# Kernel optimization log

Measured on AMD Instinct MI355X. Metric: run time of the kernel, lower is better.

## Reference

```python
import jax, jax.numpy as jnp
import numpy as np

N_NODES = 20000
N_EDGES = 320000
N_GRAPHS = 512
HEADS1 = 10
C1 = 78   # per-head out channels of gcn1
C2 = 100  # out channels of gcn2 (heads=1)
NEG_SLOPE = 0.2


def setup_inputs() -> dict:
    key = jax.random.key(0)
    ks = jax.random.split(key, 16)
    glorot = lambda k, shp: jax.random.normal(k, shp, jnp.float32) * np.sqrt(2.0 / (shp[0] + shp[-1]))
    x = jax.random.normal(ks[0], (N_NODES, 78), jnp.float32)
    edge_index = jax.random.randint(ks[1], (2, N_EDGES), 0, N_NODES, jnp.int64)
    batch = jnp.sort(jax.random.randint(ks[2], (N_NODES,), 0, N_GRAPHS, jnp.int64))
    return {
        "x": x,
        "edge_index": edge_index,
        "batch": batch,
        "num_graphs": N_GRAPHS,
        "W1": glorot(ks[3], (78, HEADS1 * C1)),
        "a_src1": glorot(ks[4], (HEADS1, C1)),
        "a_dst1": glorot(ks[5], (HEADS1, C1)),
        "b1": jnp.zeros((HEADS1 * C1,), jnp.float32),
        "W2": glorot(ks[6], (HEADS1 * C1, C2)),
        "a_src2": glorot(ks[7], (1, C2)),
        "a_dst2": glorot(ks[8], (1, C2)),
        "b2": jnp.zeros((C2,), jnp.float32),
        "Wg": glorot(ks[9], (C2, C2)),
        "bg": jnp.zeros((C2,), jnp.float32),
    }


def gat_conv(x, src, dst, W, a_src, a_dst, b, heads, out_ch):
    """PyG-style GATConv (concat=True, add_self_loops already applied, eval mode)."""
    N = x.shape[0]
    h = (x @ W).reshape(N, heads, out_ch)          # [N,H,C]
    alpha_s = jnp.einsum('nhc,hc->nh', h, a_src)   # [N,H]
    alpha_d = jnp.einsum('nhc,hc->nh', h, a_dst)
    e = jax.nn.leaky_relu(alpha_s[src] + alpha_d[dst], NEG_SLOPE)  # [E,H]
    # segment softmax over destination nodes
    m = jax.ops.segment_max(e, dst, num_segments=N)                # [N,H]
    e = jnp.exp(e - m[dst])
    denom = jax.ops.segment_sum(e, dst, num_segments=N)
    alpha = e / (denom[dst] + 1e-16)                               # [E,H]
    out = jax.ops.segment_sum(h[src] * alpha[:, :, None], dst, num_segments=N)
    return out.reshape(N, heads * out_ch) + b


def reference(x, edge_index, batch, num_graphs, W1, a_src1, a_dst1, b1,
              W2, a_src2, a_dst2, b2, Wg, bg):
    N = x.shape[0]
    # add self loops (PyG GATConv default)
    loops = jnp.arange(N, dtype=edge_index.dtype)
    src = jnp.concatenate([edge_index[0], loops])
    dst = jnp.concatenate([edge_index[1], loops])
    h = gat_conv(x, src, dst, W1, a_src1, a_dst1, b1, HEADS1, C1)   # [N,780]
    h = jax.nn.elu(h)
    h = gat_conv(h, src, dst, W2, a_src2, a_dst2, b2, 1, C2)        # [N,100]
    h = jax.nn.relu(h)
    g = jax.ops.segment_max(h, batch, num_segments=num_graphs)      # [G,100] global max pool
    g = jax.nn.relu(g @ Wg + bg)
    return g
```

## Files before the change

### kernel.cpp

```cpp
#include <hip/hip_runtime.h>
#include <hip/hip_bf16.h>

#define N_NODES  20000
#define N_EDGES  320000
#define E_TOT    (N_EDGES + N_NODES)
#define N_GRAPHS 512
#define H1 10
#define C1 78
#define F1 780
#define C2 100
#define NEG_SLOPE 0.2f
#define KSPLIT 5
#define K1PAD 96
#define K2PAD 800
#define K2CHUNK 160
#define AP1 104
#define AP2 40
#define HP 12

typedef short bf16x8 __attribute__((ext_vector_type(8)));
typedef float f32x4 __attribute__((ext_vector_type(4)));
typedef _Float16 half2v __attribute__((ext_vector_type(2)));
typedef unsigned short ushort_t;

__device__ __forceinline__ float bf_lo(unsigned int u) { return __uint_as_float(u << 16); }
__device__ __forceinline__ float bf_hi(unsigned int u) { return __uint_as_float(u & 0xFFFF0000u); }
__device__ __forceinline__ ushort_t f2b(float v) {
  __hip_bfloat16 b = __float2bfloat16(v);
  return *reinterpret_cast<ushort_t*>(&b);
}
__device__ __forceinline__ ushort_t f2h(float v) {
  _Float16 h = (_Float16)v;
  return *reinterpret_cast<ushort_t*>(&h);
}
__device__ __forceinline__ float lrelu(float v) { return (v > 0.f) ? v : NEG_SLOPE * v; }
__device__ __forceinline__ float dot2h(unsigned int a, unsigned int b, float c) {
  union { unsigned int u; half2v v; } A, B;
  A.u = a; B.u = b;
  return __builtin_amdgcn_fdot2(A.v, B.v, c, false);
}


#define PR0 (2 * H1 * C1)
#define PR1 (H1 * 80 * K1PAD)
#define PR2 (112 * K2PAD)
#define PR3 (N_NODES * (K2PAD - F1))
#define PR4 (N_NODES * 40)
#define PRT (PR0 + PR1 + PR2 + PR3 + PR4)
#define NB_CNT ((E_TOT + 255) / 256)
#define NB_PREP ((PRT + 255) / 256)

__global__ void k_cntprep(const int* __restrict__ ei,
                          const float* __restrict__ W1, const float* __restrict__ a_src,
                          const float* __restrict__ a_dst, const float* __restrict__ W2,
                          const float* __restrict__ x,
                          int* __restrict__ cnt,
                          float* __restrict__ Vs, float* __restrict__ Vd,
                          ushort_t* __restrict__ W1t, ushort_t* __restrict__ W2t,
                          ushort_t* __restrict__ hab, ushort_t* __restrict__ xhf) {
  if (blockIdx.x < NB_CNT) {
    int e = blockIdx.x * 256 + threadIdx.x;
    if (e >= E_TOT) return;
    int dst = (e < N_EDGES) ? ei[N_EDGES + e] : (e - N_EDGES);
    atomicAdd(&cnt[dst], 1);
    return;
  }
  int t = (blockIdx.x - NB_CNT) * 256 + threadIdx.x;
  if (t < PR0) {
    int which = (t >= H1 * C1) ? 1 : 0;
    int r = t - which * H1 * C1;
    int h = r / C1, k = r - h * C1;
    const float* a = which ? a_dst : a_src;
    float s = 0.f;
    for (int c = 0; c < C1; c++) s += W1[(size_t)k * F1 + h * C1 + c] * a[h * C1 + c];
    (which ? Vd : Vs)[h * C1 + k] = s;
    return;
  }
  t -= PR0;
  if (t < PR1) {
    int h = t / (80 * K1PAD);
    int rem = t - h * 80 * K1PAD;
    int c = rem / K1PAD, k = rem - c * K1PAD;
    float v = (c < C1 && k < C1) ? W1[(size_t)k * F1 + h * C1 + c] : 0.f;
    W1t[t] = f2b(v);
    return;
  }
  t -= PR1;
  if (t < PR2) {
    int c = t / K2PAD, k = t - c * K2PAD;
    float v = (c < C2 && k < F1) ? W2[(size_t)k * C2 + c] : 0.f;
    W2t[t] = f2b(v);
    return;
  }
  t -= PR2;
  if (t < PR3) {
    int n = t / (K2PAD - F1), j = t - n * (K2PAD - F1);
    hab[(size_t)n * K2PAD + F1 + j] = 0;
    return;
  }
  t -= PR3;
  if (t < PR4) {
    int n = t / 40, c2 = t - n * 40;
    ushort2 o;
    if (c2 < 39) { o.x = f2h(x[(size_t)n * C1 + 2 * c2]); o.y = f2h(x[(size_t)n * C1 + 2 * c2 + 1]); }
    else         { o.x = 0; o.y = 0; }
    *(ushort2*)(xhf + (size_t)n * 80 + 2 * c2) = o;
  }
}


__global__ __launch_bounds__(1024) void k_scanalpha(const int* __restrict__ cnt,
                                                    int* __restrict__ offs,
                                                    const float* __restrict__ x,
                                                    const float* __restrict__ Vs,
                                                    const float* __restrict__ Vd,
                                                    float* __restrict__ asb,
                                                    float* __restrict__ adb) {
  if (blockIdx.x == 0) {
    const int PER = 20;
    int t = threadIdx.x;
    int lane = t & 63, wv = t >> 6;
    int base = t * PER;
    int raw[PER];
    const int4* c4 = (const int4*)(cnt + base);
#pragma unroll
    for (int q = 0; q < 5; q++) {
      int4 v = c4[q];
      raw[4 * q] = v.x; raw[4 * q + 1] = v.y; raw[4 * q + 2] = v.z; raw[4 * q + 3] = v.w;
    }
    int loc[PER];
    int run = 0;
#pragma unroll
    for (int k = 0; k < PER; k++) {
      int idx = base + k;
      run += (idx < N_NODES) ? raw[k] : 0;
      loc[k] = run;
    }
    int total = run;
    int sc = total;
#pragma unroll
    for (int o = 1; o < 64; o <<= 1) {
      int u = __shfl_up(sc, o);
      if (lane >= o) sc += u;
    }
    __shared__ int ws[16];
    if (lane == 63) ws[wv] = sc;
    __syncthreads();
    if (t == 0) {
      int r = 0;
#pragma unroll
      for (int i = 0; i < 16; i++) { int v = ws[i]; ws[i] = r; r += v; }
    }
    __syncthreads();
    int excl = ws[wv] + sc - total;
#pragma unroll
    for (int k = 0; k < PER; k++) {
      int idx = base + k;
      if (idx < N_NODES) offs[idx + 1] = excl + loc[k];
    }
    if (t == 0) offs[0] = 0;
    return;
  }

  __shared__ float sVs[H1 * C1], sVd[H1 * C1];
  for (int i = threadIdx.x; i < H1 * C1; i += 1024) { sVs[i] = Vs[i]; sVd[i] = Vd[i]; }
  __syncthreads();
  int t = (blockIdx.x - 1) * 1024 + threadIdx.x;
  if (t >= N_NODES * H1) return;
  int n = t / H1, h = t - n * H1;
  const float2* row = (const float2*)(x + (size_t)n * C1);
  const float2* vs2 = (const float2*)(sVs + h * C1);
  const float2* vd2 = (const float2*)(sVd + h * C1);
  float s0 = 0.f, s1 = 0.f;
#pragma unroll 13
  for (int i = 0; i < C1 / 2; i++) {
    float2 v = row[i];
    float2 a = vs2[i];
    float2 b = vd2[i];
    s0 += v.x * a.x + v.y * a.y;
    s1 += v.x * b.x + v.y * b.y;
  }
  asb[(size_t)n * HP + h] = s0;
  adb[(size_t)n * HP + h] = s1;
}

__global__ void k_scatter(const int* __restrict__ ei, const int* __restrict__ offs,
                          int* __restrict__ cursor, int* __restrict__ srcs,
                          int* __restrict__ dsts) {
  int e = blockIdx.x * blockDim.x + threadIdx.x;
  if (e >= E_TOT) return;
  int src, dst;
  if (e < N_EDGES) { src = ei[e]; dst = ei[N_EDGES + e]; }
  else             { src = dst = e - N_EDGES; }
  int pos = offs[dst] + atomicAdd(&cursor[dst], 1);
  srcs[pos] = src;
  dsts[pos] = dst;
}


__global__ void k_ex1(const float* __restrict__ asb, const float* __restrict__ adb,
                      const int* __restrict__ srcs, const int* __restrict__ dsts,
                      ushort_t* __restrict__ ex1t) {
  int e = blockIdx.x * blockDim.x + threadIdx.x;
  if (e >= E_TOT) return;
  int s = srcs[e], d = dsts[e];
  const float* pa = asb + (size_t)s * HP;
  const float* pd = adb + (size_t)d * HP;
  float4 a0 = *(const float4*)pa, a1 = *(const float4*)(pa + 4);
  float2 a2 = *(const float2*)(pa + 8);
  float4 d0 = *(const float4*)pd, d1 = *(const float4*)(pd + 4);
  float2 d2 = *(const float2*)(pd + 8);
  float r[10];
  r[0] = __expf(lrelu(a0.x + d0.x)); r[1] = __expf(lrelu(a0.y + d0.y));
  r[2] = __expf(lrelu(a0.z + d0.z)); r[3] = __expf(lrelu(a0.w + d0.w));
  r[4] = __expf(lrelu(a1.x + d1.x)); r[5] = __expf(lrelu(a1.y + d1.y));
  r[6] = __expf(lrelu(a1.z + d1.z)); r[7] = __expf(lrelu(a1.w + d1.w));
  r[8] = __expf(lrelu(a2.x + d2.x)); r[9] = __expf(lrelu(a2.y + d2.y));
#pragma unroll
  for (int h = 0; h < H1; h++) ex1t[(size_t)h * E_TOT + e] = f2h(r[h]);
}


__global__ __launch_bounds__(256) void k_aggv5(const ushort_t* __restrict__ xhf,
                                               const ushort_t* __restrict__ ex1t,
                                               const int* __restrict__ offs,
                                               const int* __restrict__ srcs,
                                               ushort_t* __restrict__ xb) {
  int wid = (blockIdx.x * 256 + threadIdx.x) >> 6;
  int lane = threadIdx.x & 63;
  if (wid >= N_NODES) return;
  int n = wid;
  int beg = __builtin_amdgcn_readfirstlane(offs[n]);
  int end = __builtin_amdgcn_readfirstlane(offs[n + 1]);

  float acc0[H1] = {}, acc1[H1] = {}, sum[H1] = {};
  const unsigned int ONES = 0x3C003C00u;

  for (int e0 = beg & ~1; e0 < end; e0 += 2) {
    unsigned int m = 0xFFFFFFFFu;
    if (e0 < beg) m &= 0xFFFF0000u;
    if (e0 + 1 >= end) m &= 0x0000FFFFu;
    int s0 = srcs[e0], s1 = srcs[e0 + 1];
    unsigned int w[H1];
#pragma unroll
    for (int h = 0; h < H1; h++)
      w[h] = *(const unsigned int*)(ex1t + (size_t)h * E_TOT + e0);
    unsigned int xv0 = 0, xv1 = 0;
    if (lane < 39) {
      xv0 = *(const unsigned int*)(xhf + (size_t)s0 * 80 + 2 * lane);
      xv1 = *(const unsigned int*)(xhf + (size_t)s1 * 80 + 2 * lane);
    }
    unsigned int xA = __builtin_amdgcn_perm(xv1, xv0, 0x05040100u) & m;
    unsigned int xB = __builtin_amdgcn_perm(xv1, xv0, 0x07060302u) & m;
    unsigned int on = ONES & m;
#pragma unroll
    for (int h = 0; h < H1; h++) {
      acc0[h] = dot2h(w[h], xA, acc0[h]);
      acc1[h] = dot2h(w[h], xB, acc1[h]);
      sum[h]  = dot2h(w[h], on, sum[h]);
    }
  }

  if (lane < 48) {
    int colu = (lane < 39) ? 2 * lane : C1 + 2 * (lane - 39);
#pragma unroll
    for (int h = 0; h < H1; h++) {
      float iv = 1.f / (sum[h] + 1e-16f);
      ushort2 o;
      if (lane < 39) { o.x = f2b(acc0[h] * iv); o.y = f2b(acc1[h] * iv); }
      else           { o.x = 0; o.y = 0; }
      *(ushort2*)(xb + ((size_t)h * N_NODES + n) * K1PAD + colu) = o;
    }
  }
}


__global__ __launch_bounds__(256) void k_bgemm_m(const ushort_t* __restrict__ xb,
                                                 const ushort_t* __restrict__ W1t,
                                                 const float* __restrict__ b1,
                                                 ushort_t* __restrict__ hab) {
  __shared__ ushort_t sA[64 * AP1];
  __shared__ ushort_t sB[80 * AP1];
  int h = blockIdx.y;
  int m0 = blockIdx.x * 64;
  int tid = threadIdx.x;

  for (int i = tid; i < 64 * 12; i += 256) {
    int r = i / 12, cx = i - r * 12;
    uint4 v = make_uint4(0, 0, 0, 0);
    int m = m0 + r;
    if (m < N_NODES) v = *(const uint4*)(xb + ((size_t)h * N_NODES + m) * K1PAD + cx * 8);
    *(uint4*)(sA + r * AP1 + cx * 8) = v;
  }
  for (int i = tid; i < 80 * 12; i += 256) {
    int c = i / 12, cx = i - c * 12;
    uint4 v = *(const uint4*)(W1t + ((size_t)h * 80 + c) * K1PAD + cx * 8);
    *(uint4*)(sB + c * AP1 + cx * 8) = v;
  }
  __syncthreads();

  int w = tid >> 6, l = tid & 63;
  int rb = l & 15, g = l >> 4;
  f32x4 acc[5] = {};
  const ushort_t* pa = sA + (w * 16 + rb) * AP1 + g * 8;
#pragma unroll
  for (int k0 = 0; k0 < K1PAD; k0 += 32) {
    bf16x8 a = *(const bf16x8*)(pa + k0);
#pragma unroll
    for (int ct = 0; ct < 5; ct++) {
      bf16x8 b = *(const bf16x8*)(sB + (ct * 16 + rb) * AP1 + k0 + g * 8);
      acc[ct] = __builtin_amdgcn_mfma_f32_16x16x32_bf16(a, b, acc[ct], 0, 0, 0);
    }
  }

  int mrow = m0 + w * 16 + g * 4;
#pragma unroll
  for (int ct = 0; ct < 5; ct++) {
    int col = ct * 16 + rb;
    if (col >= C1) continue;
    float bias = b1[h * C1 + col];
#pragma unroll
    for (int r = 0; r < 4; r++) {
      int m = mrow + r;
      if (m >= N_NODES) continue;
      float v = acc[ct][r] + bias;
      v = (v > 0.f) ? v : (__expf(v) - 1.f);
      hab[(size_t)m * K2PAD + h * C1 + col] = f2b(v);
    }
  }
}


__global__ __launch_bounds__(256) void k_gemm2m(const ushort_t* __restrict__ hab,
                                                const ushort_t* __restrict__ W2t,
                                                float* __restrict__ part) {
  __shared__ ushort_t sA[64 * AP2];
  __shared__ ushort_t sB[112 * AP2];
  int m0 = blockIdx.x * 64;
  int kz = blockIdx.y * K2CHUNK;
  int tid = threadIdx.x;
  int w = tid >> 6, l = tid & 63;
  int rb = l & 15, g = l >> 4;
  f32x4 acc[7] = {};

  for (int ks = 0; ks < K2CHUNK; ks += 32) {
    int kbase = kz + ks;
    {
      int r = tid >> 2, cx = tid & 3;
      uint4 v = make_uint4(0, 0, 0, 0);
      int m = m0 + r;
      if (m < N_NODES) v = *(const uint4*)(hab + (size_t)m * K2PAD + kbase + cx * 8);
      *(uint4*)(sA + r * AP2 + cx * 8) = v;
    }
    for (int i = tid; i < 112 * 4; i += 256) {
      int c = i >> 2, cx = i & 3;
      uint4 v = *(const uint4*)(W2t + (size_t)c * K2PAD + kbase + cx * 8);
      *(uint4*)(sB + c * AP2 + cx * 8) = v;
    }
    __syncthreads();
    bf16x8 a = *(const bf16x8*)(sA + (w * 16 + rb) * AP2 + g * 8);
#pragma unroll
    for (int ct = 0; ct < 7; ct++) {
      bf16x8 b = *(const bf16x8*)(sB + (ct * 16 + rb) * AP2 + g * 8);
      acc[ct] = __builtin_amdgcn_mfma_f32_16x16x32_bf16(a, b, acc[ct], 0, 0, 0);
    }
    __syncthreads();
  }

  float* P = part + (size_t)blockIdx.y * N_NODES * C2;
  int mrow = m0 + w * 16 + g * 4;
#pragma unroll
  for (int ct = 0; ct < 7; ct++) {
    int col = ct * 16 + rb;
    if (col >= C2) continue;
#pragma unroll
    for (int r = 0; r < 4; r++) {
      int m = mrow + r;
      if (m < N_NODES) P[(size_t)m * C2 + col] = acc[ct][r];
    }
  }
}


__global__ __launch_bounds__(256) void k_redalpha(const float* __restrict__ part,
                                                  const float* __restrict__ a_src,
                                                  const float* __restrict__ a_dst,
                                                  ushort_t* __restrict__ z2b,
                                                  float* __restrict__ as2,
                                                  float* __restrict__ ad2) {
  int wid = (blockIdx.x * 256 + threadIdx.x) >> 6;
  int lane = threadIdx.x & 63;
  if (wid >= N_NODES) return;
  float ps = 0.f, pd = 0.f;
  if (lane < C2 / 2) {
    float2 s = make_float2(0.f, 0.f);
#pragma unroll
    for (int c = 0; c < KSPLIT; c++) {
      float2 v = *(const float2*)(part + (size_t)c * N_NODES * C2 + (size_t)wid * C2 + 2 * lane);
      s.x += v.x; s.y += v.y;
    }
    ushort2 o; o.x = f2b(s.x); o.y = f2b(s.y);
    *(ushort2*)(z2b + (size_t)wid * C2 + 2 * lane) = o;
    ps = s.x * a_src[2 * lane] + s.y * a_src[2 * lane + 1];
    pd = s.x * a_dst[2 * lane] + s.y * a_dst[2 * lane + 1];
  }
#pragma unroll
  for (int o = 32; o; o >>= 1) { ps += __shfl_xor(ps, o); pd += __shfl_xor(pd, o); }
  if (lane == 0) { as2[wid] = ps; ad2[wid] = pd; }
}


__global__ __launch_bounds__(256) void k_gat2v4(const ushort_t* __restrict__ z2b,
                                                const float* __restrict__ as2,
                                                const float* __restrict__ ad2,
                                                const int* __restrict__ offs,
                                                const int* __restrict__ srcs,
                                                const float* __restrict__ b2,
                                                const int* __restrict__ batch,
                                                unsigned int* __restrict__ pool) {
  int wid = (blockIdx.x * 256 + threadIdx.x) >> 6;
  int lane = threadIdx.x & 63;
  if (wid >= N_NODES) return;
  int n = wid;
  int beg = offs[n], deg = offs[n + 1] - beg;
  float adn = ad2[n];
  const unsigned int* zrow = (const unsigned int*)z2b;

  float acc0 = 0.f, acc1 = 0.f, sum = 0.f;

  for (int j = 0; j < deg; j += 8) {
    int sj[8]; bool vj[8];
#pragma unroll
    for (int q = 0; q < 8; q++) {
      int jj = j + q;
      vj[q] = jj < deg;
      sj[q] = srcs[vj[q] ? beg + jj : beg];
    }
    float p[8];
#pragma unroll
    for (int q = 0; q < 8; q++) {
      float pv = __expf(lrelu(as2[sj[q]] + adn));
      p[q] = vj[q] ? pv : 0.f;
    }
    unsigned int z[8] = {0, 0, 0, 0, 0, 0, 0, 0};
    if (lane < C2 / 2) {
#pragma unroll
      for (int q = 0; q < 8; q++) z[q] = zrow[(size_t)sj[q] * (C2 / 2) + lane];
    }
#pragma unroll
    for (int q = 0; q < 8; q++) {
      acc0 += p[q] * bf_lo(z[q]);
      acc1 += p[q] * bf_hi(z[q]);
      sum += p[q];
    }
  }

  if (lane < C2 / 2) {
    float iv = 1.f / (sum + 1e-16f);
    float v0 = fmaxf(acc0 * iv + b2[2 * lane], 0.f);
    float v1 = fmaxf(acc1 * iv + b2[2 * lane + 1], 0.f);
    int g = batch[n];
    atomicMax(&pool[g * C2 + 2 * lane], __float_as_uint(v0));
    atomicMax(&pool[g * C2 + 2 * lane + 1], __float_as_uint(v1));
  }
}


__global__ __launch_bounds__(128) void k_head(const float* __restrict__ pool,
                                              const float* __restrict__ Wg,
                                              const float* __restrict__ bg,
                                              float* __restrict__ out) {
  __shared__ float row[C2];
  int g = blockIdx.x;
  if (threadIdx.x < C2) row[threadIdx.x] = pool[g * C2 + threadIdx.x];
  __syncthreads();
  int c = threadIdx.x;
  if (c < C2) {
    float acc = bg[c];
    for (int k = 0; k < C2; k++) acc += row[k] * Wg[k * C2 + c];
    out[g * C2 + c] = fmaxf(acc, 0.f);
  }
}


extern "C" void kernel_launch(void* const* d_in, const int* in_sizes, int n_in,
                              void* d_out, int out_size, void* d_ws, size_t ws_size,
                              hipStream_t stream) {
  const float* x      = (const float*)d_in[0];
  const int*   ei     = (const int*)d_in[1];
  const int*   batch  = (const int*)d_in[2];
  const float* W1     = (const float*)d_in[4];
  const float* a_src1 = (const float*)d_in[5];
  const float* a_dst1 = (const float*)d_in[6];
  const float* b1     = (const float*)d_in[7];
  const float* W2     = (const float*)d_in[8];
  const float* a_src2 = (const float*)d_in[9];
  const float* a_dst2 = (const float*)d_in[10];
  const float* b2     = (const float*)d_in[11];
  const float* Wg     = (const float*)d_in[12];
  const float* bg     = (const float*)d_in[13];
  float* out = (float*)d_out;

  char* w = (char*)d_ws;
  size_t off = 0;
  auto alloc = [&](size_t bytes) -> void* {
    void* p = w + off;
    off += (bytes + 255) & ~(size_t)255;
    return p;
  };

  ushort_t* xb   = (ushort_t*)alloc((size_t)H1 * N_NODES * K1PAD * 2);
  ushort_t* hab  = (ushort_t*)alloc((size_t)N_NODES * K2PAD * 2);
  float* part    = (float*)alloc((size_t)KSPLIT * N_NODES * C2 * 4);
  float* asb     = (float*)alloc((size_t)N_NODES * HP * 4);
  float* adb     = (float*)alloc((size_t)N_NODES * HP * 4);
  ushort_t* ex1t = (ushort_t*)alloc((size_t)H1 * E_TOT * 2);
  ushort_t* xhf  = (ushort_t*)alloc((size_t)N_NODES * 80 * 2);
  float* Vs      = (float*)alloc((size_t)H1 * C1 * 4);
  float* Vd      = (float*)alloc((size_t)H1 * C1 * 4);
  ushort_t* W1t  = (ushort_t*)alloc((size_t)H1 * 80 * K1PAD * 2);
  ushort_t* W2t  = (ushort_t*)alloc((size_t)112 * K2PAD * 2);
  int* cnt           = (int*)alloc((size_t)N_NODES * 4);
  int* cursor        = (int*)alloc((size_t)N_NODES * 4);
  unsigned int* pool = (unsigned int*)alloc((size_t)N_GRAPHS * C2 * 4);
  size_t zspan = (size_t)((char*)(pool + (size_t)N_GRAPHS * C2) - (char*)cnt);
  int* offs   = (int*)alloc((size_t)(N_NODES + 1) * 4);
  int* srcs   = (int*)alloc((size_t)E_TOT * 4);
  int* dsts   = (int*)alloc((size_t)E_TOT * 4);

  float* as2    = (float*)xb;
  float* ad2    = as2 + N_NODES;
  ushort_t* z2b = (ushort_t*)(ad2 + N_NODES);

  hipMemsetAsync(cnt, 0, zspan, stream);

  k_cntprep<<<NB_CNT + NB_PREP, 256, 0, stream>>>(ei, W1, a_src1, a_dst1, W2, x,
                                                  cnt, Vs, Vd, W1t, W2t, hab, xhf);
  k_scanalpha<<<1 + (N_NODES * H1 + 1023) / 1024, 1024, 0, stream>>>(cnt, offs, x, Vs, Vd,
                                                                     asb, adb);
  k_scatter<<<(E_TOT + 255) / 256, 256, 0, stream>>>(ei, offs, cursor, srcs, dsts);
  k_ex1<<<(E_TOT + 255) / 256, 256, 0, stream>>>(asb, adb, srcs, dsts, ex1t);
  k_aggv5<<<(N_NODES + 3) / 4, 256, 0, stream>>>(xhf, ex1t, offs, srcs, xb);
  k_bgemm_m<<<dim3((N_NODES + 63) / 64, H1), 256, 0, stream>>>(xb, W1t, b1, hab);

  k_gemm2m<<<dim3((N_NODES + 63) / 64, KSPLIT), 256, 0, stream>>>(hab, W2t, part);
  k_redalpha<<<(N_NODES + 3) / 4, 256, 0, stream>>>(part, a_src2, a_dst2, z2b, as2, ad2);
  k_gat2v4<<<(N_NODES + 3) / 4, 256, 0, stream>>>(z2b, as2, ad2, offs, srcs, b2, batch, pool);
  k_head<<<N_GRAPHS, 128, 0, stream>>>((const float*)pool, Wg, bg, out);
}
```

Baseline: 255.5 us.

## Fuse layer-1 GEMM, ELU, layer-2 GEMM and attention logits into one kernel

```diff
diff --git a/kernel.cpp b/kernel.cpp
--- a/kernel.cpp
+++ b/kernel.cpp
@@ -10,12 +10,11 @@
 #define F1 780
 #define C2 100
 #define NEG_SLOPE 0.2f
-#define KSPLIT 5
 #define K1PAD 96
 #define K2PAD 800
-#define K2CHUNK 160
 #define AP1 104
 #define AP2 40
+#define HAP 808
 #define HP 12
 
 typedef short bf16x8 __attribute__((ext_vector_type(8)));
@@ -44,9 +43,8 @@
 #define PR0 (2 * H1 * C1)
 #define PR1 (H1 * 80 * K1PAD)
 #define PR2 (112 * K2PAD)
-#define PR3 (N_NODES * (K2PAD - F1))
 #define PR4 (N_NODES * 40)
-#define PRT (PR0 + PR1 + PR2 + PR3 + PR4)
+#define PRT (PR0 + PR1 + PR2 + PR4)
 #define NB_CNT ((E_TOT + 255) / 256)
 #define NB_PREP ((PRT + 255) / 256)
 
@@ -57,7 +55,7 @@
                           int* __restrict__ cnt,
                           float* __restrict__ Vs, float* __restrict__ Vd,
                           ushort_t* __restrict__ W1t, ushort_t* __restrict__ W2t,
-                          ushort_t* __restrict__ hab, ushort_t* __restrict__ xhf) {
+                          ushort_t* __restrict__ xhf) {
   if (blockIdx.x < NB_CNT) {
     int e = blockIdx.x * 256 + threadIdx.x;
     if (e >= E_TOT) return;
@@ -93,12 +91,6 @@
     return;
   }
   t -= PR2;
-  if (t < PR3) {
-    int n = t / (K2PAD - F1), j = t - n * (K2PAD - F1);
-    hab[(size_t)n * K2PAD + F1 + j] = 0;
-    return;
-  }
-  t -= PR3;
   if (t < PR4) {
     int n = t / 40, c2 = t - n * 40;
     ushort2 o;
@@ -184,9 +176,11 @@
   adb[(size_t)n * HP + h] = s1;
 }
 
-__global__ void k_scatter(const int* __restrict__ ei, const int* __restrict__ offs,
-                          int* __restrict__ cursor, int* __restrict__ srcs,
-                          int* __restrict__ dsts) {
+
+__global__ void k_scatterex(const int* __restrict__ ei, const int* __restrict__ offs,
+                            int* __restrict__ cursor,
+                            const float* __restrict__ asb, const float* __restrict__ adb,
+                            int* __restrict__ srcs, ushort_t* __restrict__ ex1t) {
   int e = blockIdx.x * blockDim.x + threadIdx.x;
   if (e >= E_TOT) return;
   int src, dst;
@@ -194,18 +188,8 @@
   else             { src = dst = e - N_EDGES; }
   int pos = offs[dst] + atomicAdd(&cursor[dst], 1);
   srcs[pos] = src;
-  dsts[pos] = dst;
-}
-
-
-__global__ void k_ex1(const float* __restrict__ asb, const float* __restrict__ adb,
-                      const int* __restrict__ srcs, const int* __restrict__ dsts,
-                      ushort_t* __restrict__ ex1t) {
-  int e = blockIdx.x * blockDim.x + threadIdx.x;
-  if (e >= E_TOT) return;
-  int s = srcs[e], d = dsts[e];
-  const float* pa = asb + (size_t)s * HP;
-  const float* pd = adb + (size_t)d * HP;
+  const float* pa = asb + (size_t)src * HP;
+  const float* pd = adb + (size_t)dst * HP;
   float4 a0 = *(const float4*)pa, a1 = *(const float4*)(pa + 4);
   float2 a2 = *(const float2*)(pa + 8);
   float4 d0 = *(const float4*)pd, d1 = *(const float4*)(pd + 4);
@@ -217,7 +201,7 @@
   r[6] = __expf(lrelu(a1.z + d1.z)); r[7] = __expf(lrelu(a1.w + d1.w));
   r[8] = __expf(lrelu(a2.x + d2.x)); r[9] = __expf(lrelu(a2.y + d2.y));
 #pragma unroll
-  for (int h = 0; h < H1; h++) ex1t[(size_t)h * E_TOT + e] = f2h(r[h]);
+  for (int h = 0; h < H1; h++) ex1t[(size_t)h * E_TOT + pos] = f2h(r[h]);
 }
 
 
@@ -275,138 +259,112 @@
 }
 
 
-__global__ __launch_bounds__(256) void k_bgemm_m(const ushort_t* __restrict__ xb,
+__global__ __launch_bounds__(256) void k_fused12(const ushort_t* __restrict__ xb,
                                                  const ushort_t* __restrict__ W1t,
                                                  const float* __restrict__ b1,
-                                                 ushort_t* __restrict__ hab) {
-  __shared__ ushort_t sA[64 * AP1];
-  __shared__ ushort_t sB[80 * AP1];
-  int h = blockIdx.y;
+                                                 const ushort_t* __restrict__ W2t,
+                                                 const float* __restrict__ a_src,
+                                                 const float* __restrict__ a_dst,
+                                                 ushort_t* __restrict__ z2b,
+                                                 float* __restrict__ as2,
+                                                 float* __restrict__ ad2) {
+  __shared__ ushort_t sHA[64 * HAP];
+  __shared__ ushort_t sS[80 * AP1];
+  __shared__ ushort_t sXB[64 * AP1];
   int m0 = blockIdx.x * 64;
-  int tid = threadIdx.x;
-
-  for (int i = tid; i < 64 * 12; i += 256) {
-    int r = i / 12, cx = i - r * 12;
-    uint4 v = make_uint4(0, 0, 0, 0);
-    int m = m0 + r;
-    if (m < N_NODES) v = *(const uint4*)(xb + ((size_t)h * N_NODES + m) * K1PAD + cx * 8);
-    *(uint4*)(sA + r * AP1 + cx * 8) = v;
-  }
-  for (int i = tid; i < 80 * 12; i += 256) {
-    int c = i / 12, cx = i - c * 12;
-    uint4 v = *(const uint4*)(W1t + ((size_t)h * 80 + c) * K1PAD + cx * 8);
-    *(uint4*)(sB + c * AP1 + cx * 8) = v;
-  }
-  __syncthreads();
-
-  int w = tid >> 6, l = tid & 63;
-  int rb = l & 15, g = l >> 4;
-  f32x4 acc[5] = {};
-  const ushort_t* pa = sA + (w * 16 + rb) * AP1 + g * 8;
-#pragma unroll
-  for (int k0 = 0; k0 < K1PAD; k0 += 32) {
-    bf16x8 a = *(const bf16x8*)(pa + k0);
-#pragma unroll
-    for (int ct = 0; ct < 5; ct++) {
-      bf16x8 b = *(const bf16x8*)(sB + (ct * 16 + rb) * AP1 + k0 + g * 8);
-      acc[ct] = __builtin_amdgcn_mfma_f32_16x16x32_bf16(a, b, acc[ct], 0, 0, 0);
-    }
-  }
-
-  int mrow = m0 + w * 16 + g * 4;
-#pragma unroll
-  for (int ct = 0; ct < 5; ct++) {
-    int col = ct * 16 + rb;
-    if (col >= C1) continue;
-    float bias = b1[h * C1 + col];
-#pragma unroll
-    for (int r = 0; r < 4; r++) {
-      int m = mrow + r;
-      if (m >= N_NODES) continue;
-      float v = acc[ct][r] + bias;
-      v = (v > 0.f) ? v : (__expf(v) - 1.f);
-      hab[(size_t)m * K2PAD + h * C1 + col] = f2b(v);
-    }
-  }
-}
-
-
-__global__ __launch_bounds__(256) void k_gemm2m(const ushort_t* __restrict__ hab,
-                                                const ushort_t* __restrict__ W2t,
-                                                float* __restrict__ part) {
-  __shared__ ushort_t sA[64 * AP2];
-  __shared__ ushort_t sB[112 * AP2];
-  int m0 = blockIdx.x * 64;
-  int kz = blockIdx.y * K2CHUNK;
   int tid = threadIdx.x;
   int w = tid >> 6, l = tid & 63;
   int rb = l & 15, g = l >> 4;
-  f32x4 acc[7] = {};
-
-  for (int ks = 0; ks < K2CHUNK; ks += 32) {
-    int kbase = kz + ks;
-    {
-      int r = tid >> 2, cx = tid & 3;
+
+  for (int i = tid; i < 64 * 28; i += 256) {
+    int r = i / 28, c = i - r * 28;
+    sHA[r * HAP + F1 + c] = 0;
+  }
+
+  for (int h = 0; h < H1; h++) {
+    __syncthreads();
+    for (int i = tid; i < 64 * 12; i += 256) {
+      int r = i / 12, cx = i - r * 12;
       uint4 v = make_uint4(0, 0, 0, 0);
       int m = m0 + r;
-      if (m < N_NODES) v = *(const uint4*)(hab + (size_t)m * K2PAD + kbase + cx * 8);
-      *(uint4*)(sA + r * AP2 + cx * 8) = v;
-    }
+      if (m < N_NODES) v = *(const uint4*)(xb + ((size_t)h * N_NODES + m) * K1PAD + cx * 8);
+      *(uint4*)(sXB + r * AP1 + cx * 8) = v;
+    }
+    for (int i = tid; i < 80 * 12; i += 256) {
+      int c = i / 12, cx = i - c * 12;
+      uint4 v = *(const uint4*)(W1t + ((size_t)h * 80 + c) * K1PAD + cx * 8);
+      *(uint4*)(sS + c * AP1 + cx * 8) = v;
+    }
+    __syncthreads();
+    f32x4 acc[5] = {};
+    const ushort_t* pa = sXB + (w * 16 + rb) * AP1 + g * 8;
+#pragma unroll
+    for (int k0 = 0; k0 < K1PAD; k0 += 32) {
+      bf16x8 a = *(const bf16x8*)(pa + k0);
+#pragma unroll
+      for (int ct = 0; ct < 5; ct++) {
+        bf16x8 b = *(const bf16x8*)(sS + (ct * 16 + rb) * AP1 + k0 + g * 8);
+        acc[ct] = __builtin_amdgcn_mfma_f32_16x16x32_bf16(a, b, acc[ct], 0, 0, 0);
+      }
+    }
+    int mrow_l = w * 16 + g * 4;
+#pragma unroll
+    for (int ct = 0; ct < 5; ct++) {
+      int col = ct * 16 + rb;
+      if (col >= C1) continue;
+      float bias = b1[h * C1 + col];
+#pragma unroll
+      for (int r = 0; r < 4; r++) {
+        float v = acc[ct][r] + bias;
+        v = (v > 0.f) ? v : (__expf(v) - 1.f);
+        sHA[(mrow_l + r) * HAP + h * C1 + col] = f2b(v);
+      }
+    }
+  }
+  __syncthreads();
+
+  f32x4 acc2[7] = {};
+  for (int ks = 0; ks < 25; ks++) {
+    if (ks) __syncthreads();
     for (int i = tid; i < 112 * 4; i += 256) {
       int c = i >> 2, cx = i & 3;
-      uint4 v = *(const uint4*)(W2t + (size_t)c * K2PAD + kbase + cx * 8);
-      *(uint4*)(sB + c * AP2 + cx * 8) = v;
+      uint4 v = *(const uint4*)(W2t + (size_t)c * K2PAD + ks * 32 + cx * 8);
+      *(uint4*)(sS + c * AP2 + cx * 8) = v;
     }
     __syncthreads();
-    bf16x8 a = *(const bf16x8*)(sA + (w * 16 + rb) * AP2 + g * 8);
+    bf16x8 a = *(const bf16x8*)(sHA + (w * 16 + rb) * HAP + ks * 32 + g * 8);
 #pragma unroll
     for (int ct = 0; ct < 7; ct++) {
-      bf16x8 b = *(const bf16x8*)(sB + (ct * 16 + rb) * AP2 + g * 8);
-      acc[ct] = __builtin_amdgcn_mfma_f32_16x16x32_bf16(a, b, acc[ct], 0, 0, 0);
-    }
-    __syncthreads();
-  }
-
-  float* P = part + (size_t)blockIdx.y * N_NODES * C2;
-  int mrow = m0 + w * 16 + g * 4;
+      bf16x8 b = *(const bf16x8*)(sS + (ct * 16 + rb) * AP2 + g * 8);
+      acc2[ct] = __builtin_amdgcn_mfma_f32_16x16x32_bf16(a, b, acc2[ct], 0, 0, 0);
+    }
+  }
+
+  float asv[7], adv[7];
 #pragma unroll
   for (int ct = 0; ct < 7; ct++) {
     int col = ct * 16 + rb;
-    if (col >= C2) continue;
-#pragma unroll
-    for (int r = 0; r < 4; r++) {
-      int m = mrow + r;
-      if (m < N_NODES) P[(size_t)m * C2 + col] = acc[ct][r];
-    }
-  }
-}
-
-
-__global__ __launch_bounds__(256) void k_redalpha(const float* __restrict__ part,
-                                                  const float* __restrict__ a_src,
-                                                  const float* __restrict__ a_dst,
-                                                  ushort_t* __restrict__ z2b,
-                                                  float* __restrict__ as2,
-                                                  float* __restrict__ ad2) {
-  int wid = (blockIdx.x * 256 + threadIdx.x) >> 6;
-  int lane = threadIdx.x & 63;
-  if (wid >= N_NODES) return;
-  float ps = 0.f, pd = 0.f;
-  if (lane < C2 / 2) {
-    float2 s = make_float2(0.f, 0.f);
-#pragma unroll
-    for (int c = 0; c < KSPLIT; c++) {
-      float2 v = *(const float2*)(part + (size_t)c * N_NODES * C2 + (size_t)wid * C2 + 2 * lane);
-      s.x += v.x; s.y += v.y;
-    }
-    ushort2 o; o.x = f2b(s.x); o.y = f2b(s.y);
-    *(ushort2*)(z2b + (size_t)wid * C2 + 2 * lane) = o;
-    ps = s.x * a_src[2 * lane] + s.y * a_src[2 * lane + 1];
-    pd = s.x * a_dst[2 * lane] + s.y * a_dst[2 * lane + 1];
-  }
-#pragma unroll
-  for (int o = 32; o; o >>= 1) { ps += __shfl_xor(ps, o); pd += __shfl_xor(pd, o); }
-  if (lane == 0) { as2[wid] = ps; ad2[wid] = pd; }
+    bool cv = col < C2;
+    asv[ct] = cv ? a_src[cv ? col : 0] : 0.f;
+    adv[ct] = cv ? a_dst[cv ? col : 0] : 0.f;
+  }
+#pragma unroll
+  for (int r = 0; r < 4; r++) {
+    int m = m0 + w * 16 + g * 4 + r;
+    bool mv = m < N_NODES;
+    float ps = 0.f, pd = 0.f;
+#pragma unroll
+    for (int ct = 0; ct < 7; ct++) {
+      int col = ct * 16 + rb;
+      float z = acc2[ct][r];
+      if (col < C2 && mv) z2b[(size_t)m * C2 + col] = f2b(z);
+      ps += z * asv[ct];
+      pd += z * adv[ct];
+    }
+#pragma unroll
+    for (int o = 8; o; o >>= 1) { ps += __shfl_xor(ps, o); pd += __shfl_xor(pd, o); }
+    if (mv && rb == 0) { as2[m] = ps; ad2[m] = pd; }
+  }
 }
 
 
@@ -510,8 +468,6 @@
   };
 
   ushort_t* xb   = (ushort_t*)alloc((size_t)H1 * N_NODES * K1PAD * 2);
-  ushort_t* hab  = (ushort_t*)alloc((size_t)N_NODES * K2PAD * 2);
-  float* part    = (float*)alloc((size_t)KSPLIT * N_NODES * C2 * 4);
   float* asb     = (float*)alloc((size_t)N_NODES * HP * 4);
   float* adb     = (float*)alloc((size_t)N_NODES * HP * 4);
   ushort_t* ex1t = (ushort_t*)alloc((size_t)H1 * E_TOT * 2);
@@ -520,31 +476,27 @@
   float* Vd      = (float*)alloc((size_t)H1 * C1 * 4);
   ushort_t* W1t  = (ushort_t*)alloc((size_t)H1 * 80 * K1PAD * 2);
   ushort_t* W2t  = (ushort_t*)alloc((size_t)112 * K2PAD * 2);
+  ushort_t* z2b  = (ushort_t*)alloc((size_t)N_NODES * C2 * 2);
+  float* as2     = (float*)alloc((size_t)N_NODES * 4);
+  float* ad2     = (float*)alloc((size_t)N_NODES * 4);
   int* cnt           = (int*)alloc((size_t)N_NODES * 4);
   int* cursor        = (int*)alloc((size_t)N_NODES * 4);
   unsigned int* pool = (unsigned int*)alloc((size_t)N_GRAPHS * C2 * 4);
   size_t zspan = (size_t)((char*)(pool + (size_t)N_GRAPHS * C2) - (char*)cnt);
   int* offs   = (int*)alloc((size_t)(N_NODES + 1) * 4);
   int* srcs   = (int*)alloc((size_t)E_TOT * 4);
-  int* dsts   = (int*)alloc((size_t)E_TOT * 4);
-
-  float* as2    = (float*)xb;
-  float* ad2    = as2 + N_NODES;
-  ushort_t* z2b = (ushort_t*)(ad2 + N_NODES);
 
   hipMemsetAsync(cnt, 0, zspan, stream);
 
   k_cntprep<<<NB_CNT + NB_PREP, 256, 0, stream>>>(ei, W1, a_src1, a_dst1, W2, x,
-                                                  cnt, Vs, Vd, W1t, W2t, hab, xhf);
+                                                  cnt, Vs, Vd, W1t, W2t, xhf);
   k_scanalpha<<<1 + (N_NODES * H1 + 1023) / 1024, 1024, 0, stream>>>(cnt, offs, x, Vs, Vd,
                                                                      asb, adb);
-  k_scatter<<<(E_TOT + 255) / 256, 256, 0, stream>>>(ei, offs, cursor, srcs, dsts);
-  k_ex1<<<(E_TOT + 255) / 256, 256, 0, stream>>>(asb, adb, srcs, dsts, ex1t);
+  k_scatterex<<<(E_TOT + 255) / 256, 256, 0, stream>>>(ei, offs, cursor, asb, adb,
+                                                       srcs, ex1t);
   k_aggv5<<<(N_NODES + 3) / 4, 256, 0, stream>>>(xhf, ex1t, offs, srcs, xb);
-  k_bgemm_m<<<dim3((N_NODES + 63) / 64, H1), 256, 0, stream>>>(xb, W1t, b1, hab);
-
-  k_gemm2m<<<dim3((N_NODES + 63) / 64, KSPLIT), 256, 0, stream>>>(hab, W2t, part);
-  k_redalpha<<<(N_NODES + 3) / 4, 256, 0, stream>>>(part, a_src2, a_dst2, z2b, as2, ad2);
+  k_fused12<<<(N_NODES + 63) / 64, 256, 0, stream>>>(xb, W1t, b1, W2t, a_src2, a_dst2,
+                                                     z2b, as2, ad2);
   k_gat2v4<<<(N_NODES + 3) / 4, 256, 0, stream>>>(z2b, as2, ad2, offs, srcs, b2, batch, pool);
   k_head<<<N_GRAPHS, 128, 0, stream>>>((const float*)pool, Wg, bg, out);
 }
```

New measurement: 330.1 us. +29.2%, slower.
